# Optimization experiments

Hardware: AMD Instinct MI355X
Metric: run time of the kernel (lower is better)

## Reference

```python
import jax, jax.numpy as jnp
import numpy as np

B, N, F_IN, H = 1, 4096, 256, 4
OUT_F = 256
HEAD_DIM = OUT_F // H
E_RAND = 131072  # avg degree 32
LN_EPS = 1e-5


def setup_inputs() -> dict:
    key = jax.random.key(0)
    ks = jax.random.split(key, 12)
    x = jax.random.normal(ks[0], (B, N, F_IN), jnp.float32)
    # random edges + self-loops so every softmax row has at least one unmasked entry
    src = jax.random.randint(ks[1], (E_RAND,), 0, N, dtype=jnp.int32)
    dst = jax.random.randint(ks[2], (E_RAND,), 0, N, dtype=jnp.int32)
    loops = jnp.arange(N, dtype=jnp.int32)
    edge_index = jnp.stack([jnp.concatenate([loops, src]), jnp.concatenate([loops, dst])])
    s = 1.0 / np.sqrt(F_IN)
    Wq = jax.random.uniform(ks[3], (OUT_F, F_IN), jnp.float32, -s, s)
    bq = jax.random.uniform(ks[4], (OUT_F,), jnp.float32, -s, s)
    Wk = jax.random.uniform(ks[5], (OUT_F, F_IN), jnp.float32, -s, s)
    bk = jax.random.uniform(ks[6], (OUT_F,), jnp.float32, -s, s)
    Wv = jax.random.uniform(ks[7], (OUT_F, F_IN), jnp.float32, -s, s)
    bv = jax.random.uniform(ks[8], (OUT_F,), jnp.float32, -s, s)
    ln_g = jnp.ones((OUT_F,), jnp.float32)
    ln_b = jnp.zeros((OUT_F,), jnp.float32)
    return {"x": x, "edge_index": edge_index, "Wq": Wq, "bq": bq, "Wk": Wk,
            "bk": bk, "Wv": Wv, "bv": bv, "ln_g": ln_g, "ln_b": ln_b}


def _layer_norm(y, g, b):
    mu = jnp.mean(y, axis=-1, keepdims=True)
    var = jnp.mean(jnp.square(y - mu), axis=-1, keepdims=True)
    return (y - mu) * jax.lax.rsqrt(var + LN_EPS) * g + b


def reference(x, edge_index, Wq, bq, Wk, bk, Wv, bv, ln_g, ln_b):
    b, n, f_in = x.shape
    out_f = Wq.shape[0]
    hd = out_f // H
    # linear projections -> [b, H, n, hd]
    Q = (x @ Wq.T + bq).reshape(b, n, H, hd).transpose(0, 2, 1, 3)
    K = (x @ Wk.T + bk).reshape(b, n, H, hd).transpose(0, 2, 1, 3)
    V = (x @ Wv.T + bv).reshape(b, n, H, hd).transpose(0, 2, 1, 3)
    scores = jnp.einsum('bhnd,bhmd->bhnm', Q, K) / jnp.sqrt(jnp.float32(hd))
    # adjacency mask: same for every batch/head (torch scatters identically per b,h)
    adj = jnp.zeros((n, n), bool).at[edge_index[0], edge_index[1]].set(True)
    scores = jnp.where(adj, scores, -jnp.inf)
    attn = jax.nn.softmax(scores, axis=-1)  # dropout = identity (eval)
    out = jnp.einsum('bhnm,bhmd->bhnd', attn, V)
    out = out.transpose(0, 2, 1, 3).reshape(b, n, out_f)
    out = out + x if f_in == out_f else out  # residual
    out = _layer_norm(out, ln_g, ln_b)
    return (out, attn)
```

## Files before the change

### kernel.cpp

```cpp
#include <hip/hip_runtime.h>
#include <stdint.h>

#define NNODES 4096
#define FDIM 256
#define NH 4
#define HD 64
#define MWORDS 128
#define SCAP 512
#define TOTROWS (NH * NNODES)
#define ROW4 (NNODES / 4)
#define R0 6144
#define R1 14336
#define FB3 24576
#define FB4 32768
#define FB5 8192

typedef float f4 __attribute__((ext_vector_type(4)));

__device__ __forceinline__ void fill_one_nt(f4* __restrict__ base, size_t beg, size_t end,
                                            int fid, int t)
{
    size_t i = beg + (size_t)fid * 256 + t;
    if (i < end) {
        f4 z = {0.f, 0.f, 0.f, 0.f};
        f4* p = base + i;
        asm volatile("global_store_dwordx4 %0, %1, off sc0 sc1 nt"
                     :: "v"(p), "v"(z) : "memory");
    }
}

__global__ __launch_bounds__(256) void k_prep(
    const float* __restrict__ Wq, const float* __restrict__ Wk,
    const float* __restrict__ Wv, float* __restrict__ Wt,
    const int* __restrict__ ei, int E, uint32_t* __restrict__ mask)
{
    __shared__ float tile[32][33];
    int t = threadIdx.x;
    if (blockIdx.x < 192) {
        int mat = blockIdx.x >> 6;
        int within = blockIdx.x & 63;
        int c0 = (within & 7) * 32, r0 = (within >> 3) * 32;
        const float* W = mat == 0 ? Wq : (mat == 1 ? Wk : Wv);
        float* dst = Wt + (size_t)mat * FDIM * FDIM;
        int tx = t & 31, ty = t >> 5;
        for (int i = ty; i < 32; i += 8)
            tile[i][tx] = W[(size_t)(r0 + i) * FDIM + c0 + tx];
        __syncthreads();
        for (int i = ty; i < 32; i += 8)
            dst[(size_t)(c0 + i) * FDIM + r0 + tx] = tile[tx][i];
    } else {
        int e = (blockIdx.x - 192) * 256 + t;
        if (e < E) {
            int r = ei[e];
            int c = ei[E + e];
            atomicOr(&mask[(size_t)r * MWORDS + (c >> 5)], 1u << (c & 31));
        }
    }
}

#define TN 16
__global__ __launch_bounds__(256) void k_qkv_fill(
    const float* __restrict__ x, const float* __restrict__ Wt,
    const float* __restrict__ bq, const float* __restrict__ bk, const float* __restrict__ bv,
    float* __restrict__ qkv, float* __restrict__ attn)
{
    int t = threadIdx.x;
    if (blockIdx.x >= 3 * (NNODES / TN)) {
        fill_one_nt((f4*)attn, 0, (size_t)R0 * ROW4, blockIdx.x - 3 * (NNODES / TN), t);
        return;
    }
    int mat = blockIdx.x >> 8;
    int n0 = (blockIdx.x & 255) * TN;
    const float* W = Wt + (size_t)mat * FDIM * FDIM;
    const float* bias = mat == 0 ? bq : (mat == 1 ? bk : bv);
    float* dst = qkv + (size_t)mat * NNODES * FDIM;
    __shared__ float xl[TN][FDIM + 4];
    for (int f = t; f < TN * (FDIM / 4); f += 256) {
        int n = f >> 6, c4 = f & 63;
        float4 v = ((const float4*)(x + (size_t)(n0 + n) * FDIM))[c4];
        *(float4*)&xl[n][c4 * 4] = v;
    }
    __syncthreads();
    float acc[TN];
    #pragma unroll
    for (int n = 0; n < TN; ++n) acc[n] = 0.f;
    for (int k4 = 0; k4 < FDIM / 4; ++k4) {
        float w0 = W[(size_t)(k4 * 4 + 0) * FDIM + t];
        float w1 = W[(size_t)(k4 * 4 + 1) * FDIM + t];
        float w2 = W[(size_t)(k4 * 4 + 2) * FDIM + t];
        float w3 = W[(size_t)(k4 * 4 + 3) * FDIM + t];
        #pragma unroll
        for (int n = 0; n < TN; ++n) {
            float4 xv = *(const float4*)&xl[n][k4 * 4];
            acc[n] = fmaf(w0, xv.x, acc[n]);
            acc[n] = fmaf(w1, xv.y, acc[n]);
            acc[n] = fmaf(w2, xv.z, acc[n]);
            acc[n] = fmaf(w3, xv.w, acc[n]);
        }
    }
    float bb = bias[t];
    #pragma unroll
    for (int n = 0; n < TN; ++n)
        dst[(size_t)(n0 + n) * FDIM + t] = acc[n] + bb;
}

__global__ __launch_bounds__(256) void k_attn_fill(
    const float* __restrict__ qkv, const uint32_t* __restrict__ mask,
    const float* __restrict__ x, const float* __restrict__ ln_g, const float* __restrict__ ln_b,
    float* __restrict__ out, float* __restrict__ stats, float* __restrict__ attn)
{
    int t = threadIdx.x;
    if (blockIdx.x >= NNODES) {
        fill_one_nt((f4*)attn, (size_t)R0 * ROW4, (size_t)R1 * ROW4, blockIdx.x - NNODES, t);
        return;
    }

    const float* Q = qkv;
    const float* K = qkv + (size_t)NNODES * FDIM;
    const float* V = qkv + 2 * (size_t)NNODES * FDIM;

    __shared__ float q_lds[FDIM];
    __shared__ uint32_t mrow[MWORDS];
    __shared__ unsigned short list[NNODES];
    __shared__ float sv[NH][SCAP];
    __shared__ float red0[NH], red1[NH];
    __shared__ int cnt_s;

    int n = blockIdx.x;
    int h = t >> 6, lane = t & 63;

    q_lds[t] = Q[(size_t)n * FDIM + t];
    float xv = x[(size_t)n * FDIM + t];
    if (t < MWORDS) mrow[t] = mask[(size_t)n * MWORDS + t];
    __syncthreads();

    if (t < 64) {
        int total = 0;
        for (int r = 0; r < 2; ++r) {
            int w = r * 64 + t;
            uint32_t bits = mrow[w];
            int c = __popc(bits);
            int scan = c;
            #pragma unroll
            for (int off = 1; off < 64; off <<= 1) {
                int u = __shfl_up(scan, off);
                if (t >= off) scan += u;
            }
            int base = total + scan - c;
            while (bits) {
                int b = __ffs(bits) - 1;
                list[base++] = (unsigned short)(w * 32 + b);
                bits &= bits - 1;
            }
            total += __shfl(scan, 63);
        }
        if (t == 0) cnt_s = total;
    }
    __syncthreads();
    int cnt = cnt_s;

    const float4* qh = (const float4*)(q_lds + h * HD);

    float mi = -INFINITY, li = 0.f;
    for (int i = lane; i < cnt; i += 64) {
        int m = list[i];
        const float4* kp = (const float4*)(K + (size_t)m * FDIM + h * HD);
        float s = 0.f;
        #pragma unroll
        for (int j = 0; j < HD / 4; ++j) {
            float4 a = qh[j], b = kp[j];
            s += a.x * b.x + a.y * b.y + a.z * b.z + a.w * b.w;
        }
        s *= 0.125f;
        if (i < SCAP) sv[h][i] = s;
        float nm = fmaxf(mi, s);
        li = li * __expf(mi - nm) + __expf(s - nm);
        mi = nm;
    }
    #pragma unroll
    for (int off = 32; off; off >>= 1) {
        float mo = __shfl_xor(mi, off);
        float lo = __shfl_xor(li, off);
        float nm = fmaxf(mi, mo);
        float ea = (nm == -INFINITY) ? 0.f : __expf(mi - nm);
        float eb = (nm == -INFINITY) ? 0.f : __expf(mo - nm);
        li = li * ea + lo * eb;
        mi = nm;
    }
    float M = mi;
    float Linv = 1.f / li;
    if (lane == 0) {
        stats[((size_t)h * NNODES + n) * 2 + 0] = M;
        stats[((size_t)h * NNODES + n) * 2 + 1] = Linv;
    }

    int cm = min(cnt, SCAP);
    for (int i = lane; i < cm; i += 64)
        sv[h][i] = __expf(sv[h][i] - M) * Linv;

    const float* vb = V + (size_t)h * HD + lane;
    float o0 = 0.f, o1 = 0.f, o2 = 0.f, o3 = 0.f;
    int j = 0;
    for (; j + 3 < cm; j += 4) {
        int m0 = list[j], m1 = list[j + 1], m2 = list[j + 2], m3 = list[j + 3];
        float p0 = sv[h][j], p1 = sv[h][j + 1], p2 = sv[h][j + 2], p3 = sv[h][j + 3];
        o0 = fmaf(p0, vb[(size_t)m0 * FDIM], o0);
        o1 = fmaf(p1, vb[(size_t)m1 * FDIM], o1);
        o2 = fmaf(p2, vb[(size_t)m2 * FDIM], o2);
        o3 = fmaf(p3, vb[(size_t)m3 * FDIM], o3);
    }
    for (; j < cm; ++j)
        o0 = fmaf(sv[h][j], vb[(size_t)list[j] * FDIM], o0);
    for (; j < cnt; ++j) {
        int m = list[j];
        const float4* kp = (const float4*)(K + (size_t)m * FDIM + h * HD);
        float s = 0.f;
        #pragma unroll
        for (int jj = 0; jj < HD / 4; ++jj) {
            float4 a = qh[jj], b = kp[jj];
            s += a.x * b.x + a.y * b.y + a.z * b.z + a.w * b.w;
        }
        o0 = fmaf(__expf(s * 0.125f - M) * Linv, vb[(size_t)m * FDIM], o0);
    }
    float o = (o0 + o1) + (o2 + o3);

    float y = o + xv;
    float s1 = y, s2 = y * y;
    #pragma unroll
    for (int off = 32; off; off >>= 1) {
        s1 += __shfl_xor(s1, off);
        s2 += __shfl_xor(s2, off);
    }
    if (lane == 0) { red0[h] = s1; red1[h] = s2; }
    __syncthreads();
    float ts1 = (red0[0] + red0[1]) + (red0[2] + red0[3]);
    float ts2 = (red1[0] + red1[1]) + (red1[2] + red1[3]);
    float mu = ts1 * (1.f / 256.f);
    float var = ts2 * (1.f / 256.f) - mu * mu;
    out[(size_t)n * FDIM + t] = (y - mu) * rsqrtf(var + 1e-5f) * ln_g[t] + ln_b[t];
}

__global__ __launch_bounds__(256) void k_scatter_fill(
    const int* __restrict__ ei, int E, int nsb,
    const float* __restrict__ qkv, const float* __restrict__ stats,
    float* __restrict__ attn, int rowLo, int rowHi,
    unsigned long long fillBeg, unsigned long long fillEnd)
{
    int t = threadIdx.x;
    if (blockIdx.x >= nsb) {
        fill_one_nt((f4*)attn, (size_t)fillBeg, (size_t)fillEnd, blockIdx.x - nsb, t);
        return;
    }
    int idx = blockIdx.x * 256 + t;
    if (idx >= E * NH) return;
    int e = idx >> 2;
    int h = idx & 3;
    int r = ei[e];
    int c = ei[E + e];
    int row = h * NNODES + r;
    if (row < rowLo || row >= rowHi) return;

    const float* Q = qkv;
    const float* K = qkv + (size_t)NNODES * FDIM;
    const float4* qp = (const float4*)(Q + (size_t)r * FDIM + h * HD);
    const float4* kp = (const float4*)(K + (size_t)c * FDIM + h * HD);
    float s = 0.f;
    #pragma unroll
    for (int j = 0; j < HD / 4; ++j) {
        float4 a = qp[j], b = kp[j];
        s += a.x * b.x + a.y * b.y + a.z * b.z + a.w * b.w;
    }
    float M = stats[(size_t)row * 2 + 0];
    float Linv = stats[(size_t)row * 2 + 1];
    attn[(size_t)row * NNODES + c] = __expf(s * 0.125f - M) * Linv;
}

extern "C" void kernel_launch(void* const* d_in, const int* in_sizes, int n_in,
                              void* d_out, int out_size, void* d_ws, size_t ws_size,
                              hipStream_t stream)
{
    const float* x    = (const float*)d_in[0];
    const int*   ei   = (const int*)d_in[1];
    const float* Wq   = (const float*)d_in[2];
    const float* bq   = (const float*)d_in[3];
    const float* Wk   = (const float*)d_in[4];
    const float* bk   = (const float*)d_in[5];
    const float* Wv   = (const float*)d_in[6];
    const float* bv   = (const float*)d_in[7];
    const float* ln_g = (const float*)d_in[8];
    const float* ln_b = (const float*)d_in[9];
    float* out = (float*)d_out;
    float* attn = out + (size_t)NNODES * FDIM;

    int E = in_sizes[1] / 2;

    float* Wt  = (float*)d_ws;
    float* qkv = Wt + 3 * FDIM * FDIM;
    uint32_t* mask = (uint32_t*)(qkv + 3 * (size_t)NNODES * FDIM);
    float* stats = (float*)(mask + (size_t)NNODES * MWORDS);

    hipMemsetAsync(mask, 0, (size_t)NNODES * MWORDS * sizeof(uint32_t), stream);

    int nbuild = (E + 255) / 256;
    k_prep<<<192 + nbuild, 256, 0, stream>>>(Wq, Wk, Wv, Wt, ei, E, mask);

    k_qkv_fill<<<3 * (NNODES / TN) + FB3, 256, 0, stream>>>(x, Wt, bq, bk, bv, qkv, attn);

    k_attn_fill<<<NNODES + FB4, 256, 0, stream>>>(qkv, mask, x, ln_g, ln_b, out, stats, attn);

    int nsb = (E * NH + 255) / 256;
    k_scatter_fill<<<nsb + FB5, 256, 0, stream>>>(
        ei, E, nsb, qkv, stats, attn, 0, R1,
        (unsigned long long)R1 * ROW4, (unsigned long long)TOTROWS * ROW4);

    k_scatter_fill<<<nsb, 256, 0, stream>>>(
        ei, E, nsb, qkv, stats, attn, R1, TOTROWS, 0ull, 0ull);
}
```

Baseline: 215.8 us.

## Fuse tail rows into mask-driven dense write and drop second scatter launch

The zero-fill of the 268MB attention matrix is now split across all four kernels, with a new share in k_prep. The last rows are no longer zero-filled and then scattered. Instead they are written once densely: each thread reads mask bits and computes exp scores for set columns inline. This removes the fifth kernel launch and the double write of the tail rows. The fill also switches from nontemporal inline-asm stores to plain stores, which may change cache behaviour.

```diff
diff --git a/kernel.cpp b/kernel.cpp
--- a/kernel.cpp
+++ b/kernel.cpp
@@ -9,30 +9,29 @@
 #define SCAP 512
 #define TOTROWS (NH * NNODES)
 #define ROW4 (NNODES / 4)
-#define R0 6144
-#define R1 14336
-#define FB3 24576
-#define FB4 32768
-#define FB5 8192
+#define S0 1024
+#define S1 7936
+#define RTAIL 14848
+#define FB2 ((S0) * 4)
+#define FB3 ((S1 - S0) * 4)
+#define FB4 ((RTAIL - S1) * 4)
+#define FB5 ((TOTROWS - RTAIL) * 4)
 
 typedef float f4 __attribute__((ext_vector_type(4)));
 
-__device__ __forceinline__ void fill_one_nt(f4* __restrict__ base, size_t beg, size_t end,
-                                            int fid, int t)
-{
+__device__ __forceinline__ void fill_one(f4* __restrict__ base, size_t beg, size_t end,
+                                         int fid, int t)
+{
+    f4 z = {0.f, 0.f, 0.f, 0.f};
     size_t i = beg + (size_t)fid * 256 + t;
-    if (i < end) {
-        f4 z = {0.f, 0.f, 0.f, 0.f};
-        f4* p = base + i;
-        asm volatile("global_store_dwordx4 %0, %1, off sc0 sc1 nt"
-                     :: "v"(p), "v"(z) : "memory");
-    }
+    if (i < end) base[i] = z;
 }
 
 __global__ __launch_bounds__(256) void k_prep(
     const float* __restrict__ Wq, const float* __restrict__ Wk,
     const float* __restrict__ Wv, float* __restrict__ Wt,
-    const int* __restrict__ ei, int E, uint32_t* __restrict__ mask)
+    const int* __restrict__ ei, int E, uint32_t* __restrict__ mask,
+    float* __restrict__ attn, int nbuild)
 {
     __shared__ float tile[32][33];
     int t = threadIdx.x;
@@ -48,13 +47,15 @@
         __syncthreads();
         for (int i = ty; i < 32; i += 8)
             dst[(size_t)(c0 + i) * FDIM + r0 + tx] = tile[tx][i];
-    } else {
+    } else if (blockIdx.x < 192 + nbuild) {
         int e = (blockIdx.x - 192) * 256 + t;
         if (e < E) {
             int r = ei[e];
             int c = ei[E + e];
             atomicOr(&mask[(size_t)r * MWORDS + (c >> 5)], 1u << (c & 31));
         }
+    } else {
+        fill_one((f4*)attn, 0, (size_t)S0 * ROW4, blockIdx.x - 192 - nbuild, t);
     }
 }
 
@@ -66,7 +67,8 @@
 {
     int t = threadIdx.x;
     if (blockIdx.x >= 3 * (NNODES / TN)) {
-        fill_one_nt((f4*)attn, 0, (size_t)R0 * ROW4, blockIdx.x - 3 * (NNODES / TN), t);
+        fill_one((f4*)attn, (size_t)S0 * ROW4, (size_t)S1 * ROW4,
+                 blockIdx.x - 3 * (NNODES / TN), t);
         return;
     }
     int mat = blockIdx.x >> 8;
@@ -111,7 +113,7 @@
 {
     int t = threadIdx.x;
     if (blockIdx.x >= NNODES) {
-        fill_one_nt((f4*)attn, (size_t)R0 * ROW4, (size_t)R1 * ROW4, blockIdx.x - NNODES, t);
+        fill_one((f4*)attn, (size_t)S1 * ROW4, (size_t)RTAIL * ROW4, blockIdx.x - NNODES, t);
         return;
     }
 
@@ -240,17 +242,52 @@
     out[(size_t)n * FDIM + t] = (y - mu) * rsqrtf(var + 1e-5f) * ln_g[t] + ln_b[t];
 }
 
-__global__ __launch_bounds__(256) void k_scatter_fill(
+__global__ __launch_bounds__(256) void k_scatter_tailfill(
     const int* __restrict__ ei, int E, int nsb,
     const float* __restrict__ qkv, const float* __restrict__ stats,
-    float* __restrict__ attn, int rowLo, int rowHi,
-    unsigned long long fillBeg, unsigned long long fillEnd)
+    const uint32_t* __restrict__ mask, float* __restrict__ attn)
 {
     int t = threadIdx.x;
+    const float* Q = qkv;
+    const float* K = qkv + (size_t)NNODES * FDIM;
+
     if (blockIdx.x >= nsb) {
-        fill_one_nt((f4*)attn, (size_t)fillBeg, (size_t)fillEnd, blockIdx.x - nsb, t);
+        int f = blockIdx.x - nsb;
+        int row = RTAIL + (f >> 2);
+        int q = f & 3;
+        int h = row >> 12, n = row & 4095;
+        __shared__ float qh[HD];
+        __shared__ uint32_t mw[32];
+        __shared__ float Ms, Ls;
+        if (t < HD) qh[t] = Q[(size_t)n * FDIM + h * HD + t];
+        else if (t < HD + 32) mw[t - HD] = mask[(size_t)n * MWORDS + q * 32 + (t - HD)];
+        else if (t == HD + 32) { Ms = stats[(size_t)row * 2]; Ls = stats[(size_t)row * 2 + 1]; }
+        __syncthreads();
+        int c0 = t * 4;
+        uint32_t nib = (mw[c0 >> 5] >> (c0 & 31)) & 0xFu;
+        f4 v = {0.f, 0.f, 0.f, 0.f};
+        if (nib) {
+            float M = Ms, Linv = Ls;
+            int cbase = q * 1024 + c0;
+            #pragma unroll
+            for (int j = 0; j < 4; ++j) {
+                if ((nib >> j) & 1u) {
+                    const float4* kp = (const float4*)(K + (size_t)(cbase + j) * FDIM + h * HD);
+                    float s = 0.f;
+                    #pragma unroll
+                    for (int q4 = 0; q4 < HD / 4; ++q4) {
+                        float4 a = *(const float4*)&qh[q4 * 4];
+                        float4 b = kp[q4];
+                        s += a.x * b.x + a.y * b.y + a.z * b.z + a.w * b.w;
+                    }
+                    v[j] = __expf(s * 0.125f - M) * Linv;
+                }
+            }
+        }
+        *(f4*)(attn + (size_t)row * NNODES + q * 1024 + c0) = v;
         return;
     }
+
     int idx = blockIdx.x * 256 + t;
     if (idx >= E * NH) return;
     int e = idx >> 2;
@@ -258,10 +295,8 @@
     int r = ei[e];
     int c = ei[E + e];
     int row = h * NNODES + r;
-    if (row < rowLo || row >= rowHi) return;
-
-    const float* Q = qkv;
-    const float* K = qkv + (size_t)NNODES * FDIM;
+    if (row >= RTAIL) return;
+
     const float4* qp = (const float4*)(Q + (size_t)r * FDIM + h * HD);
     const float4* kp = (const float4*)(K + (size_t)c * FDIM + h * HD);
     float s = 0.f;
@@ -302,17 +337,12 @@
     hipMemsetAsync(mask, 0, (size_t)NNODES * MWORDS * sizeof(uint32_t), stream);
 
     int nbuild = (E + 255) / 256;
-    k_prep<<<192 + nbuild, 256, 0, stream>>>(Wq, Wk, Wv, Wt, ei, E, mask);
+    k_prep<<<192 + nbuild + FB2, 256, 0, stream>>>(Wq, Wk, Wv, Wt, ei, E, mask, attn, nbuild);
 
     k_qkv_fill<<<3 * (NNODES / TN) + FB3, 256, 0, stream>>>(x, Wt, bq, bk, bv, qkv, attn);
 
     k_attn_fill<<<NNODES + FB4, 256, 0, stream>>>(qkv, mask, x, ln_g, ln_b, out, stats, attn);
 
     int nsb = (E * NH + 255) / 256;
-    k_scatter_fill<<<nsb + FB5, 256, 0, stream>>>(
-        ei, E, nsb, qkv, stats, attn, 0, R1,
-        (unsigned long long)R1 * ROW4, (unsigned long long)TOTROWS * ROW4);
-
-    k_scatter_fill<<<nsb, 256, 0, stream>>>(
-        ei, E, nsb, qkv, stats, attn, R1, TOTROWS, 0ull, 0ull);
-}
+    k_scatter_tailfill<<<nsb + FB5, 256, 0, stream>>>(ei, E, nsb, qkv, stats, mask, attn);
+}
```

Measured after the change: 195.1 us. -9.6%, faster.
